# Optimization experiments

Measured on AMD Instinct MI355X. Metric: run time of the kernel, lower is better.

Reference implementation:

```python
import jax, jax.numpy as jnp
import numpy as np

BANDWITH = 10.0  # matches init kwarg `bandwith`


def setup_inputs() -> dict:
    key = jax.random.key(0)
    kx, ky = jax.random.split(key)
    X = jax.random.normal(kx, (8192, 128), dtype=jnp.float32)
    Y = jax.random.normal(ky, (8192, 128), dtype=jnp.float32)
    return {"X": X, "Y": Y}


def reference(X, Y):
    # Z = vstack([X, Y]) : [N+M, d]
    Z = jnp.concatenate([X, Y], axis=0)
    # squared euclidean cdist: ||zi||^2 + ||zj||^2 - 2 zi.zj  (clamped >= 0)
    sq = jnp.sum(Z * Z, axis=-1)  # [N+M]
    d2 = sq[:, None] + sq[None, :] - 2.0 * jnp.matmul(Z, Z.T)
    d2 = jnp.maximum(d2, 0.0)
    # RBF kernel; the original's [None,...].sum(dim=0) over a single bandwidth is identity
    K = jnp.exp(-d2 / (2.0 * BANDWITH ** 2))  # [N+M, N+M]
    n = X.shape[0]
    XX = jnp.mean(K[:n, :n])
    XY = jnp.mean(K[:n, n:])
    YY = jnp.mean(K[n:, n:])
    return XX - 2.0 * XY + YY
```

## Files before the change

### kernel.cpp

```cpp
#include <hip/hip_runtime.h>
#include <math.h>

#define TD 128
#define BT 64
#define TB 128

typedef _Float16 half8 __attribute__((ext_vector_type(8)));
typedef _Float16 half2v __attribute__((ext_vector_type(2)));
typedef float f32x4 __attribute__((ext_vector_type(4)));

#define C2f   (-0.0072134752044448f)
#define M2C2f (0.0144269504088896f)

#if __has_builtin(__builtin_amdgcn_exp2f)
#define EXP2F(x) __builtin_amdgcn_exp2f(x)
#else
#define EXP2F(x) exp2f(x)
#endif

__device__ __forceinline__ void gload16(const void* g, void* l) {
    __builtin_amdgcn_global_load_lds(
        (const __attribute__((address_space(1))) void*)g,
        (__attribute__((address_space(3))) void*)l, 16, 0, 0);
}

__global__ __launch_bounds__(256) void cvt_norms_kernel(const float* __restrict__ X,
                                                        const float* __restrict__ Y,
                                                        int n, int tot,
                                                        _Float16* __restrict__ Z16,
                                                        float* __restrict__ En) {
    const int wid  = (blockIdx.x * 256 + threadIdx.x) >> 6;
    const int lane = threadIdx.x & 63;
    if (wid >= tot) return;
    const float* row = (wid < n) ? (X + (size_t)wid * TD) : (Y + (size_t)(wid - n) * TD);
    float2 v = *reinterpret_cast<const float2*>(row + lane * 2);
    _Float16 hx = (_Float16)v.x;
    _Float16 hy = (_Float16)v.y;
    half2v h2 = {hx, hy};
    *reinterpret_cast<half2v*>(Z16 + (size_t)wid * TD + lane * 2) = h2;
    float fx = (float)hx, fy = (float)hy;
    float s = fmaf(fx, fx, fy * fy);
#pragma unroll
    for (int off = 32; off > 0; off >>= 1) s += __shfl_down(s, off, 64);
    if (lane == 0) En[wid] = EXP2F(C2f * s);
}

__global__ __launch_bounds__(256) void mmd_mfma_kernel(const _Float16* __restrict__ Z16,
                                                       const float* __restrict__ En,
                                                       double* __restrict__ partials,
                                                       int n, int m, int T) {
    __shared__ char sAB[2 * TB * 256];
    __shared__ float sred[4];

    const int t = blockIdx.x;
    double bguess = (2.0 * T + 1.0 -
                     sqrt((2.0 * T + 1.0) * (2.0 * T + 1.0) - 8.0 * (double)t)) * 0.5;
    int bi = (int)bguess;
    if (bi < 0) bi = 0;
    if (bi > T - 1) bi = T - 1;
    while ((bi + 1) * T - ((bi + 1) * bi) / 2 <= t) ++bi;
    while (bi * T - (bi * (bi - 1)) / 2 > t) --bi;
    const int bj = bi + (t - (bi * T - (bi * (bi - 1)) / 2));

    const int tid = threadIdx.x;
    const int l = tid & 63;
    const int w = tid >> 6;

    {
        const _Float16* gA = Z16 + (size_t)bi * TB * TD;
        const _Float16* gB = Z16 + (size_t)bj * TB * TD;
        const int rl = l >> 4;
        const int sl = l & 15;
#pragma unroll
        for (int c = 0; c < 8; ++c) {
            const int ci = c * 4 + w;
            const int r  = ci * 4 + rl;
            const int src = sl ^ (r & 7);
            gload16(gA + (size_t)r * TD + src * 8, sAB + ci * 1024);
            gload16(gB + (size_t)r * TD + src * 8, sAB + 32768 + ci * 1024);
        }
    }
    __syncthreads();

    const int wrow = (w >> 1) * 64;
    const int wcol = (w & 1) * 64;
    const int lr = l & 15;
    const int kq = l >> 4;

    f32x4 acc[4][4];
#pragma unroll
    for (int i = 0; i < 4; ++i)
#pragma unroll
        for (int j = 0; j < 4; ++j) acc[i][j] = (f32x4){0.f, 0.f, 0.f, 0.f};

    const char* pA = sAB;
    const char* pB = sAB + 32768;
    const int swz = lr & 7;

#pragma unroll
    for (int ks = 0; ks < 4; ++ks) {
        half8 af[4], bf[4];
#pragma unroll
        for (int f = 0; f < 4; ++f) {
            const int slot = (ks * 4 + kq) ^ swz;
            af[f] = *reinterpret_cast<const half8*>(pA + (wrow + f * 16 + lr) * 256 + slot * 16);
            bf[f] = *reinterpret_cast<const half8*>(pB + (wcol + f * 16 + lr) * 256 + slot * 16);
        }
#pragma unroll
        for (int i = 0; i < 4; ++i)
#pragma unroll
            for (int j = 0; j < 4; ++j)
                acc[i][j] = __builtin_amdgcn_mfma_f32_16x16x32_f16(af[i], bf[j], acc[i][j], 0, 0, 0);
    }

    float Ei[4][4];
    float Ej[4];
#pragma unroll
    for (int i = 0; i < 4; ++i)
#pragma unroll
        for (int r = 0; r < 4; ++r)
            Ei[i][r] = En[bi * TB + wrow + i * 16 + kq * 4 + r];
#pragma unroll
    for (int j = 0; j < 4; ++j)
        Ej[j] = En[bj * TB + wcol + j * 16 + lr];

    float s = 0.f;
#pragma unroll
    for (int j = 0; j < 4; ++j) {
        float sj0 = 0.f, sj1 = 0.f;
#pragma unroll
        for (int i = 0; i < 4; ++i) {
#pragma unroll
            for (int r = 0; r < 4; ++r) {
                float e = EXP2F(M2C2f * acc[i][j][r]);
                if (r & 1) sj1 = fmaf(Ei[i][r], e, sj1);
                else       sj0 = fmaf(Ei[i][r], e, sj0);
            }
        }
        s = fmaf(Ej[j], sj0 + sj1, s);
    }

#pragma unroll
    for (int off = 32; off > 0; off >>= 1) s += __shfl_down(s, off, 64);
    if (l == 0) sred[w] = s;
    __syncthreads();
    if (tid == 0) {
        double wa = (bi * TB < n) ? (1.0 / (double)n) : (-1.0 / (double)m);
        double wb = (bj * TB < n) ? (1.0 / (double)n) : (-1.0 / (double)m);
        double wgt = wa * wb * ((bi == bj) ? 1.0 : 2.0);
        partials[t] = wgt * (double)(sred[0] + sred[1] + sred[2] + sred[3]);
    }
}

__global__ __launch_bounds__(256) void norms_kernel(const float* __restrict__ X,
                                                    const float* __restrict__ Y,
                                                    int n, int tot,
                                                    float* __restrict__ norms) {
    int r = blockIdx.x * 256 + threadIdx.x;
    if (r >= tot) return;
    const float* row = (r < n) ? (X + (size_t)r * TD) : (Y + (size_t)(r - n) * TD);
    float s = 0.f;
#pragma unroll
    for (int k = 0; k < TD; k += 4) {
        float4 v = *reinterpret_cast<const float4*>(row + k);
        s = fmaf(v.x, v.x, s); s = fmaf(v.y, v.y, s);
        s = fmaf(v.z, v.z, s); s = fmaf(v.w, v.w, s);
    }
    norms[r] = s;
}

__global__ __launch_bounds__(256, 2) void mmd_tile_kernel(const float* __restrict__ X,
                                                          const float* __restrict__ Y,
                                                          const float* __restrict__ norms,
                                                          double* __restrict__ partials,
                                                          int n, int m, int T) {
    __shared__ float sA[TD][BT];
    __shared__ float sB[TD][BT];
    __shared__ float sred[4];

    const int t = blockIdx.x;
    double bguess = (2.0 * T + 1.0 -
                     sqrt((2.0 * T + 1.0) * (2.0 * T + 1.0) - 8.0 * (double)t)) * 0.5;
    int bi = (int)bguess;
    if (bi < 0) bi = 0;
    if (bi > T - 1) bi = T - 1;
    while ((bi + 1) * T - ((bi + 1) * bi) / 2 <= t) ++bi;
    while (bi * T - (bi * (bi - 1)) / 2 > t) --bi;
    const int bj = bi + (t - (bi * T - (bi * (bi - 1)) / 2));

    const int tid = threadIdx.x;
    {
        const int row = tid & 63;
        const int qb  = tid >> 6;
        const int ra = bi * BT + row;
        const int rb = bj * BT + row;
        const float* Arow = (ra < n) ? (X + (size_t)ra * TD) : (Y + (size_t)(ra - n) * TD);
        const float* Brow = (rb < n) ? (X + (size_t)rb * TD) : (Y + (size_t)(rb - n) * TD);
#pragma unroll
        for (int i = 0; i < 8; ++i) {
            const int q = qb + 4 * i;
            float4 va = *reinterpret_cast<const float4*>(Arow + 4 * q);
            sA[4 * q + 0][row] = va.x; sA[4 * q + 1][row] = va.y;
            sA[4 * q + 2][row] = va.z; sA[4 * q + 3][row] = va.w;
            float4 vb = *reinterpret_cast<const float4*>(Brow + 4 * q);
            sB[4 * q + 0][row] = vb.x; sB[4 * q + 1][row] = vb.y;
            sB[4 * q + 2][row] = vb.z; sB[4 * q + 3][row] = vb.w;
        }
    }
    __syncthreads();

    const int tx = tid & 15;
    const int ty = tid >> 4;
    float acc[4][4];
#pragma unroll
    for (int i = 0; i < 4; ++i)
#pragma unroll
        for (int j = 0; j < 4; ++j) acc[i][j] = 0.f;

#pragma unroll 16
    for (int k = 0; k < TD; ++k) {
        float4 a = *reinterpret_cast<const float4*>(&sA[k][ty * 4]);
        float4 b = *reinterpret_cast<const float4*>(&sB[k][tx * 4]);
        const float av[4] = {a.x, a.y, a.z, a.w};
        const float bv[4] = {b.x, b.y, b.z, b.w};
#pragma unroll
        for (int i = 0; i < 4; ++i)
#pragma unroll
            for (int j = 0; j < 4; ++j)
                acc[i][j] = fmaf(av[i], bv[j], acc[i][j]);
    }

    float nA[4], nB[4];
#pragma unroll
    for (int i = 0; i < 4; ++i) nA[i] = norms[bi * BT + ty * 4 + i];
#pragma unroll
    for (int j = 0; j < 4; ++j) nB[j] = norms[bj * BT + tx * 4 + j];

    const float cexp = -0.005f;
    float s = 0.f;
#pragma unroll
    for (int i = 0; i < 4; ++i)
#pragma unroll
        for (int j = 0; j < 4; ++j) {
            float d2 = fmaxf(nA[i] + nB[j] - 2.f * acc[i][j], 0.f);
            s += __expf(d2 * cexp);
        }

#pragma unroll
    for (int off = 32; off > 0; off >>= 1) s += __shfl_down(s, off, 64);
    if ((tid & 63) == 0) sred[tid >> 6] = s;
    __syncthreads();
    if (tid == 0) {
        double wa = (bi * BT < n) ? (1.0 / (double)n) : (-1.0 / (double)m);
        double wb = (bj * BT < n) ? (1.0 / (double)n) : (-1.0 / (double)m);
        double wgt = wa * wb * ((bi == bj) ? 1.0 : 2.0);
        partials[t] = wgt * (double)(sred[0] + sred[1] + sred[2] + sred[3]);
    }
}

__global__ __launch_bounds__(256) void reduce_kernel(const double* __restrict__ partials,
                                                     int npart,
                                                     float* __restrict__ out) {
    __shared__ double sd[256];
    double s = 0.0;
    for (int i = threadIdx.x; i < npart; i += 256) s += partials[i];
    sd[threadIdx.x] = s;
    __syncthreads();
    for (int off = 128; off > 0; off >>= 1) {
        if ((int)threadIdx.x < off) sd[threadIdx.x] += sd[threadIdx.x + off];
        __syncthreads();
    }
    if (threadIdx.x == 0) out[0] = (float)sd[0];
}

extern "C" void kernel_launch(void* const* d_in, const int* in_sizes, int n_in,
                              void* d_out, int out_size, void* d_ws, size_t ws_size,
                              hipStream_t stream) {
    const float* X = (const float*)d_in[0];
    const float* Y = (const float*)d_in[1];
    float* out = (float*)d_out;

    const int n = in_sizes[0] / TD;
    const int m = in_sizes[1] / TD;
    const int tot = n + m;

    const size_t z16_bytes = (size_t)tot * TD * 2;
    const size_t sn2_off   = (z16_bytes + 255) & ~(size_t)255;
    const size_t sn2_bytes = (size_t)tot * 4;
    const size_t part_off  = ((sn2_off + sn2_bytes) + 255) & ~(size_t)255;
    const int Tm = tot / TB;
    const int npart_m = Tm * (Tm + 1) / 2;
    const size_t needed = part_off + (size_t)npart_m * 8;

    if (ws_size >= needed && (tot % TB) == 0 && (n % TB) == 0) {
        _Float16* Z16 = (_Float16*)d_ws;
        float* En = (float*)((char*)d_ws + sn2_off);
        double* partials = (double*)((char*)d_ws + part_off);
        cvt_norms_kernel<<<(tot + 3) / 4, 256, 0, stream>>>(X, Y, n, tot, Z16, En);
        mmd_mfma_kernel<<<npart_m, 256, 0, stream>>>(Z16, En, partials, n, m, Tm);
        reduce_kernel<<<1, 256, 0, stream>>>(partials, npart_m, out);
    } else {
        const int T = tot / BT;
        const int npart = T * (T + 1) / 2;
        float* norms = (float*)d_ws;
        double* partials = (double*)((char*)d_ws + (((size_t)tot * 4 + 255) & ~(size_t)255));
        norms_kernel<<<(tot + 255) / 256, 256, 0, stream>>>(X, Y, n, tot, norms);
        mmd_tile_kernel<<<T * (T + 1) / 2, 256, 0, stream>>>(X, Y, norms, partials, n, m, T);
        reduce_kernel<<<1, 256, 0, stream>>>(partials, npart, out);
    }
}
```

Baseline: 79.47 us.

## Enlarge MFMA tile to 256 with 512-thread blocks and stage norms in LDS

Doubles the symmetric block tile from 128 to 256 rows and launches 512-thread blocks, with each of 8 waves computing a 128x64 sub-tile. The goal is to halve the global reloads of Z16 and the per-block overhead (fewer triangular blocks, fewer partials). The per-row exp-norm factors are now loaded asynchronously into LDS with the tiles instead of read from global memory per lane. The trade-off is about 133KB of LDS per block, which likely allows only one block per CU and leaves little room to overlap loads with compute. Diagonal tiles also get coarser.

```diff
diff --git a/kernel.cpp b/kernel.cpp
--- a/kernel.cpp
+++ b/kernel.cpp
@@ -3,7 +3,7 @@
 
 #define TD 128
 #define BT 64
-#define TB 128
+#define TB 256
 
 typedef _Float16 half8 __attribute__((ext_vector_type(8)));
 typedef _Float16 half2v __attribute__((ext_vector_type(2)));
@@ -23,6 +23,11 @@
         (const __attribute__((address_space(1))) void*)g,
         (__attribute__((address_space(3))) void*)l, 16, 0, 0);
 }
+
+#define LDS_B   65536
+#define LDS_EA  131072
+#define LDS_EB  132096
+#define LDS_RED 133120
 
 __global__ __launch_bounds__(256) void cvt_norms_kernel(const float* __restrict__ X,
                                                         const float* __restrict__ Y,
@@ -45,12 +50,11 @@
     if (lane == 0) En[wid] = EXP2F(C2f * s);
 }
 
-__global__ __launch_bounds__(256) void mmd_mfma_kernel(const _Float16* __restrict__ Z16,
-                                                       const float* __restrict__ En,
-                                                       double* __restrict__ partials,
-                                                       int n, int m, int T) {
-    __shared__ char sAB[2 * TB * 256];
-    __shared__ float sred[4];
+__global__ __launch_bounds__(512, 2) void mmd_mfma_kernel(const _Float16* __restrict__ Z16,
+                                                          const float* __restrict__ En,
+                                                          double* __restrict__ partials,
+                                                          int n, int m, int T) {
+    __shared__ char sAB[133152];
 
     const int t = blockIdx.x;
     double bguess = (2.0 * T + 1.0 -
@@ -73,68 +77,80 @@
         const int sl = l & 15;
 #pragma unroll
         for (int c = 0; c < 8; ++c) {
-            const int ci = c * 4 + w;
+            const int ci = c * 8 + w;
             const int r  = ci * 4 + rl;
-            const int src = sl ^ (r & 7);
+            const int src = sl ^ (r & 15);
             gload16(gA + (size_t)r * TD + src * 8, sAB + ci * 1024);
-            gload16(gB + (size_t)r * TD + src * 8, sAB + 32768 + ci * 1024);
-        }
-    }
-    __syncthreads();
-
-    const int wrow = (w >> 1) * 64;
-    const int wcol = (w & 1) * 64;
+            gload16(gB + (size_t)r * TD + src * 8, sAB + LDS_B + ci * 1024);
+        }
+        if (w == 0) gload16(En + bi * TB + l * 4, sAB + LDS_EA);
+        if (w == 1) gload16(En + bj * TB + l * 4, sAB + LDS_EB);
+    }
+    __syncthreads();
+
+    const int wrow = (w >> 2) * 128;
+    const int wcol = (w & 3) * 64;
     const int lr = l & 15;
     const int kq = l >> 4;
 
-    f32x4 acc[4][4];
-#pragma unroll
-    for (int i = 0; i < 4; ++i)
-#pragma unroll
-        for (int j = 0; j < 4; ++j) acc[i][j] = (f32x4){0.f, 0.f, 0.f, 0.f};
-
     const char* pA = sAB;
-    const char* pB = sAB + 32768;
-    const int swz = lr & 7;
-
-#pragma unroll
-    for (int ks = 0; ks < 4; ++ks) {
-        half8 af[4], bf[4];
-#pragma unroll
-        for (int f = 0; f < 4; ++f) {
-            const int slot = (ks * 4 + kq) ^ swz;
-            af[f] = *reinterpret_cast<const half8*>(pA + (wrow + f * 16 + lr) * 256 + slot * 16);
-            bf[f] = *reinterpret_cast<const half8*>(pB + (wcol + f * 16 + lr) * 256 + slot * 16);
-        }
-#pragma unroll
-        for (int i = 0; i < 4; ++i)
+    const char* pB = sAB + LDS_B;
+
+    f32x4 acc[8][4];
+    const f32x4 zero4 = {0.f, 0.f, 0.f, 0.f};
+
+    {
+        half8 bf[4];
+#pragma unroll
+        for (int j = 0; j < 4; ++j) {
+            const int slot = kq ^ lr;
+            bf[j] = *reinterpret_cast<const half8*>(pB + (wcol + j * 16 + lr) * 256 + slot * 16);
+        }
+#pragma unroll
+        for (int i = 0; i < 8; ++i) {
+            const int slot = kq ^ lr;
+            half8 af = *reinterpret_cast<const half8*>(pA + (wrow + i * 16 + lr) * 256 + slot * 16);
 #pragma unroll
             for (int j = 0; j < 4; ++j)
-                acc[i][j] = __builtin_amdgcn_mfma_f32_16x16x32_f16(af[i], bf[j], acc[i][j], 0, 0, 0);
-    }
-
-    float Ei[4][4];
+                acc[i][j] = __builtin_amdgcn_mfma_f32_16x16x32_f16(af, bf[j], zero4, 0, 0, 0);
+        }
+    }
+#pragma unroll
+    for (int ks = 1; ks < 4; ++ks) {
+        half8 bf[4];
+        const int slot = (ks * 4 + kq) ^ lr;
+#pragma unroll
+        for (int j = 0; j < 4; ++j)
+            bf[j] = *reinterpret_cast<const half8*>(pB + (wcol + j * 16 + lr) * 256 + slot * 16);
+#pragma unroll
+        for (int i = 0; i < 8; ++i) {
+            half8 af = *reinterpret_cast<const half8*>(pA + (wrow + i * 16 + lr) * 256 + slot * 16);
+#pragma unroll
+            for (int j = 0; j < 4; ++j)
+                acc[i][j] = __builtin_amdgcn_mfma_f32_16x16x32_f16(af, bf[j], acc[i][j], 0, 0, 0);
+        }
+    }
+
     float Ej[4];
 #pragma unroll
-    for (int i = 0; i < 4; ++i)
-#pragma unroll
-        for (int r = 0; r < 4; ++r)
-            Ei[i][r] = En[bi * TB + wrow + i * 16 + kq * 4 + r];
-#pragma unroll
     for (int j = 0; j < 4; ++j)
-        Ej[j] = En[bj * TB + wcol + j * 16 + lr];
+        Ej[j] = *reinterpret_cast<const float*>(sAB + LDS_EB + (wcol + j * 16 + lr) * 4);
+    f32x4 EiV[8];
+#pragma unroll
+    for (int i = 0; i < 8; ++i)
+        EiV[i] = *reinterpret_cast<const f32x4*>(sAB + LDS_EA + (wrow + i * 16 + kq * 4) * 4);
 
     float s = 0.f;
 #pragma unroll
     for (int j = 0; j < 4; ++j) {
         float sj0 = 0.f, sj1 = 0.f;
 #pragma unroll
-        for (int i = 0; i < 4; ++i) {
+        for (int i = 0; i < 8; ++i) {
 #pragma unroll
             for (int r = 0; r < 4; ++r) {
                 float e = EXP2F(M2C2f * acc[i][j][r]);
-                if (r & 1) sj1 = fmaf(Ei[i][r], e, sj1);
-                else       sj0 = fmaf(Ei[i][r], e, sj0);
+                if (r & 1) sj1 = fmaf(EiV[i][r], e, sj1);
+                else       sj0 = fmaf(EiV[i][r], e, sj0);
             }
         }
         s = fmaf(Ej[j], sj0 + sj1, s);
@@ -142,13 +158,17 @@
 
 #pragma unroll
     for (int off = 32; off > 0; off >>= 1) s += __shfl_down(s, off, 64);
+    float* sred = reinterpret_cast<float*>(sAB + LDS_RED);
     if (l == 0) sred[w] = s;
     __syncthreads();
     if (tid == 0) {
+        float bs = 0.f;
+#pragma unroll
+        for (int q = 0; q < 8; ++q) bs += sred[q];
         double wa = (bi * TB < n) ? (1.0 / (double)n) : (-1.0 / (double)m);
         double wb = (bj * TB < n) ? (1.0 / (double)n) : (-1.0 / (double)m);
         double wgt = wa * wb * ((bi == bj) ? 1.0 : 2.0);
-        partials[t] = wgt * (double)(sred[0] + sred[1] + sred[2] + sred[3]);
+        partials[t] = wgt * (double)bs;
     }
 }
 
@@ -176,7 +196,7 @@
                                                           int n, int m, int T) {
     __shared__ float sA[TD][BT];
     __shared__ float sB[TD][BT];
-    __shared__ float sred[4];
+    __shared__ float sredf[4];
 
     const int t = blockIdx.x;
     double bguess = (2.0 * T + 1.0 -
@@ -248,13 +268,13 @@
 
 #pragma unroll
     for (int off = 32; off > 0; off >>= 1) s += __shfl_down(s, off, 64);
-    if ((tid & 63) == 0) sred[tid >> 6] = s;
+    if ((tid & 63) == 0) sredf[tid >> 6] = s;
     __syncthreads();
     if (tid == 0) {
         double wa = (bi * BT < n) ? (1.0 / (double)n) : (-1.0 / (double)m);
         double wb = (bj * BT < n) ? (1.0 / (double)n) : (-1.0 / (double)m);
         double wgt = wa * wb * ((bi == bj) ? 1.0 : 2.0);
-        partials[t] = wgt * (double)(sred[0] + sred[1] + sred[2] + sred[3]);
+        partials[t] = wgt * (double)(sredf[0] + sredf[1] + sredf[2] + sredf[3]);
     }
 }
 
@@ -285,19 +305,19 @@
     const int tot = n + m;
 
     const size_t z16_bytes = (size_t)tot * TD * 2;
-    const size_t sn2_off   = (z16_bytes + 255) & ~(size_t)255;
-    const size_t sn2_bytes = (size_t)tot * 4;
-    const size_t part_off  = ((sn2_off + sn2_bytes) + 255) & ~(size_t)255;
+    const size_t en_off    = (z16_bytes + 255) & ~(size_t)255;
+    const size_t en_bytes  = (size_t)tot * 4;
+    const size_t part_off  = ((en_off + en_bytes) + 255) & ~(size_t)255;
     const int Tm = tot / TB;
     const int npart_m = Tm * (Tm + 1) / 2;
     const size_t needed = part_off + (size_t)npart_m * 8;
 
     if (ws_size >= needed && (tot % TB) == 0 && (n % TB) == 0) {
         _Float16* Z16 = (_Float16*)d_ws;
-        float* En = (float*)((char*)d_ws + sn2_off);
+        float* En = (float*)((char*)d_ws + en_off);
         double* partials = (double*)((char*)d_ws + part_off);
         cvt_norms_kernel<<<(tot + 3) / 4, 256, 0, stream>>>(X, Y, n, tot, Z16, En);
-        mmd_mfma_kernel<<<npart_m, 256, 0, stream>>>(Z16, En, partials, n, m, Tm);
+        mmd_mfma_kernel<<<npart_m, 512, 0, stream>>>(Z16, En, partials, n, m, Tm);
         reduce_kernel<<<1, 256, 0, stream>>>(partials, npart_m, out);
     } else {
         const int T = tot / BT;
@@ -305,7 +325,7 @@
         float* norms = (float*)d_ws;
         double* partials = (double*)((char*)d_ws + (((size_t)tot * 4 + 255) & ~(size_t)255));
         norms_kernel<<<(tot + 255) / 256, 256, 0, stream>>>(X, Y, n, tot, norms);
-        mmd_tile_kernel<<<T * (T + 1) / 2, 256, 0, stream>>>(X, Y, norms, partials, n, m, T);
+        mmd_tile_kernel<<<npart, 256, 0, stream>>>(X, Y, norms, partials, n, m, T);
         reduce_kernel<<<1, 256, 0, stream>>>(partials, npart, out);
     }
 }
```

Result: faster. 68.90 us (-13.3%).
